# Performance work log

Measured on AMD Instinct MI355X. Metric: run time of the kernel, lower is better.

The kernel has to match this reference:

```python
import jax, jax.numpy as jnp
import numpy as np

B, C, L = 256, 500, 200
D, H, NUM_ITEMS = 64, 128, 100000
BETA = 0.7
EPS = 1e-8


def _xavier(key, fan_in, fan_out):
    lim = float(np.sqrt(6.0 / (fan_in + fan_out)))
    return jax.random.uniform(key, (fan_in, fan_out), minval=-lim, maxval=lim, dtype=jnp.float32)


def setup_inputs() -> dict:
    key = jax.random.key(0)
    ks = jax.random.split(key, 12)
    inp = {
        'candidate_items': jax.random.randint(ks[0], (B, C), 0, NUM_ITEMS, dtype=jnp.int64) if jax.config.read('jax_enable_x64') else jax.random.randint(ks[0], (B, C), 0, NUM_ITEMS),
        'query_times': jax.random.uniform(ks[1], (B,), dtype=jnp.float32),
        'candidate_histories': jax.random.uniform(ks[2], (B, C, L), dtype=jnp.float32),
        'item_emb': 0.02 * jax.random.normal(ks[3], (NUM_ITEMS, D), dtype=jnp.float32),
        'base_W1': _xavier(ks[4], D, H), 'base_b1': jnp.zeros((H,), jnp.float32),
        'base_W2': _xavier(ks[5], H, H), 'base_b2': jnp.zeros((H,), jnp.float32),
        'base_W3': _xavier(ks[6], H, 1),
        'exc_W1': _xavier(ks[7], D, H), 'exc_b1': jnp.zeros((H,), jnp.float32),
        'exc_W2': _xavier(ks[8], H, H), 'exc_b2': jnp.zeros((H,), jnp.float32),
        'exc_W3': _xavier(ks[9], H, 1),
    }
    return inp


def _mlp(x, W1, b1, W2, b2, W3):
    # (Linear + Softplus) x depth, then Linear -> 1 (no bias), squeeze last dim
    h = jax.nn.softplus(x @ W1 + b1)
    h = jax.nn.softplus(h @ W2 + b2)
    return (h @ W3)[..., 0]


def reference(candidate_items, query_times, candidate_histories, item_emb,
              base_W1, base_b1, base_W2, base_b2, base_W3,
              exc_W1, exc_b1, exc_W2, exc_b2, exc_W3):
    z = item_emb[candidate_items]                                  # [B, C, D]
    mu = jax.nn.softplus(_mlp(z, base_W1, base_b1, base_W2, base_b2, base_W3)) + EPS   # [B, C]
    alpha = jax.nn.softplus(_mlp(z, exc_W1, exc_b1, exc_W2, exc_b2, exc_W3)) + EPS     # [B, C]
    q = query_times[:, None, None]                                 # [B, 1, 1]
    mask = candidate_histories < q                                 # [B, C, L]
    delta = jnp.maximum(q - candidate_histories, 0.0)              # clamp(min=0)
    h = jnp.sum(jnp.exp(-BETA * delta) * mask, axis=-1)            # [B, C]
    return mu + alpha * h
```

## Files before the change

kernel.cpp:

```cpp
#include <hip/hip_runtime.h>
#include <math.h>

#define BB 256
#define CC 500
#define LL 200
#define DD 64
#define HH 128
#define NUM_ITEMS 100000
#define BETA 0.7f
#define EPSV 1e-8f

#define TM 32
#define WPB 4
#define NTILE (NUM_ITEMS / TM)
#define BPS 1024

typedef _Float16 half8 __attribute__((ext_vector_type(8)));
typedef float floatx4 __attribute__((ext_vector_type(4)));

__device__ __forceinline__ float softplus_safe(float x) {
    float t = __expf(-fabsf(x));
    return fmaxf(x, 0.0f) + __logf(1.0f + t);
}
__device__ __forceinline__ float softplus_fast(float x) {
    return __logf(1.0f + __expf(x));
}
__device__ __forceinline__ float softplus_small(float x) {
    float z = x * x;
    float p = fmaf(fmaf(-5.2083333e-3f, z, 0.125f), z, 0.69314718f);
    return fmaf(x, 0.5f, p);
}

__global__ __launch_bounds__(256) void prep_w(
    const float* __restrict__ W1, const float* __restrict__ W2,
    const float* __restrict__ V1, const float* __restrict__ V2,
    _Float16* __restrict__ wb)
{
    int t = blockIdx.x * 256 + threadIdx.x;
    if (t >= 49152) return;
    float v;
    if (t < 8192)       { int n = t >> 6,  k = t & 63;             v = W1[k * HH + n]; }
    else if (t < 24576) { int u = t - 8192;  int n = u >> 7, k = u & 127; v = W2[k * HH + n]; }
    else if (t < 32768) { int u = t - 24576; int n = u >> 6, k = u & 63;  v = V1[k * HH + n]; }
    else                { int u = t - 32768; int n = u >> 7, k = u & 127; v = V2[k * HH + n]; }
    wb[t] = (_Float16)v;
}

__global__ __launch_bounds__(256, 4) void mlp_mfma(
    const float* __restrict__ emb, const _Float16* __restrict__ wb,
    const float* __restrict__ b1, const float* __restrict__ b2, const float* __restrict__ W3,
    const float* __restrict__ c1, const float* __restrict__ c2, const float* __restrict__ V3,
    float* __restrict__ mu, float* __restrict__ alpha)
{
    __shared__ __align__(16) _Float16 h1s[TM * HH];
    __shared__ __align__(16) float    part[TM * WPB];
    int tid  = threadIdx.x;
    int w    = tid >> 6, lane = tid & 63;
    int quad = lane >> 4, l15 = lane & 15;

    int is_exc = blockIdx.x >= BPS;
    int bslot  = blockIdx.x - (is_exc ? BPS : 0);

    const _Float16* W1t = wb + (is_exc ? 24576 : 0);
    const _Float16* W2t = wb + (is_exc ? 32768 : 8192);
    const float* B1  = is_exc ? c1 : b1;
    const float* B2  = is_exc ? c2 : b2;
    const float* W3p = is_exc ? V3 : W3;
    float* outp = is_exc ? alpha : mu;

    half8 w1f[2][2];
    half8 w2f[4][2];
    float b1v[2], b2v[2], w3v[2];
    #pragma unroll
    for (int n = 0; n < 2; ++n) {
        int j = (2 * w + n) * 16 + l15;
        b1v[n] = B1[j];
        b2v[n] = B2[j];
        w3v[n] = W3p[j];
        #pragma unroll
        for (int kt = 0; kt < 2; ++kt)
            w1f[kt][n] = *(const half8*)(W1t + j * DD + kt * 32 + quad * 8);
        #pragma unroll
        for (int kt = 0; kt < 4; ++kt)
            w2f[kt][n] = *(const half8*)(W2t + j * HH + kt * 32 + quad * 8);
    }

    #pragma unroll 1
    for (int t = bslot; t < NTILE; t += BPS) {
        half8 zf[2][2];
        #pragma unroll
        for (int mt = 0; mt < 2; ++mt) {
            const float* p = emb + (size_t)(t * TM + mt * 16 + l15) * DD + quad * 8;
            #pragma unroll
            for (int kt = 0; kt < 2; ++kt) {
                floatx4 v0 = *(const floatx4*)(p + kt * 32);
                floatx4 v1 = *(const floatx4*)(p + kt * 32 + 4);
                half8 z;
                #pragma unroll
                for (int j = 0; j < 4; ++j) {
                    z[j] = (_Float16)v0[j]; z[4 + j] = (_Float16)v1[j];
                }
                zf[mt][kt] = z;
            }
        }

        floatx4 acc1[2][2];
        #pragma unroll
        for (int n = 0; n < 2; ++n) {
            float bv = b1v[n];
            #pragma unroll
            for (int mt = 0; mt < 2; ++mt) acc1[mt][n] = (floatx4){bv, bv, bv, bv};
        }
        #pragma unroll
        for (int kt = 0; kt < 2; ++kt)
            #pragma unroll
            for (int n = 0; n < 2; ++n)
                #pragma unroll
                for (int mt = 0; mt < 2; ++mt)
                    acc1[mt][n] = __builtin_amdgcn_mfma_f32_16x16x32_f16(zf[mt][kt], w1f[kt][n], acc1[mt][n], 0, 0, 0);
        #pragma unroll
        for (int mt = 0; mt < 2; ++mt)
            #pragma unroll
            for (int n = 0; n < 2; ++n)
                #pragma unroll
                for (int r = 0; r < 4; ++r) {
                    int itq = quad * 4 + r;
                    int sw  = ((2 * w + n) * 2 + (l15 >> 3)) ^ itq;
                    h1s[(mt * 16 + itq) * HH + sw * 8 + (l15 & 7)] =
                        (_Float16)softplus_small(acc1[mt][n][r]);
                }
        __syncthreads();

        floatx4 acc2[2][2];
        #pragma unroll
        for (int n = 0; n < 2; ++n) {
            float bv = b2v[n];
            #pragma unroll
            for (int mt = 0; mt < 2; ++mt) acc2[mt][n] = (floatx4){bv, bv, bv, bv};
        }
        #pragma unroll
        for (int kt = 0; kt < 4; ++kt) {
            half8 af[2];
            #pragma unroll
            for (int mt = 0; mt < 2; ++mt)
                af[mt] = *(const half8*)(h1s + (mt * 16 + l15) * HH + (((kt * 4 + quad) ^ l15) * 8));
            #pragma unroll
            for (int n = 0; n < 2; ++n)
                #pragma unroll
                for (int mt = 0; mt < 2; ++mt)
                    acc2[mt][n] = __builtin_amdgcn_mfma_f32_16x16x32_f16(af[mt], w2f[kt][n], acc2[mt][n], 0, 0, 0);
        }
        float sacc[2][4];
        #pragma unroll
        for (int mt = 0; mt < 2; ++mt)
            #pragma unroll
            for (int r = 0; r < 4; ++r) sacc[mt][r] = 0.0f;
        #pragma unroll
        for (int n = 0; n < 2; ++n) {
            float w3 = w3v[n];
            #pragma unroll
            for (int mt = 0; mt < 2; ++mt)
                #pragma unroll
                for (int r = 0; r < 4; ++r)
                    sacc[mt][r] += softplus_fast(acc2[mt][n][r]) * w3;
        }
        #pragma unroll
        for (int mt = 0; mt < 2; ++mt)
            #pragma unroll
            for (int r = 0; r < 4; ++r) {
                float s = sacc[mt][r];
                s += __shfl_xor(s, 1, 64);
                s += __shfl_xor(s, 2, 64);
                s += __shfl_xor(s, 4, 64);
                s += __shfl_xor(s, 8, 64);
                if (l15 == 0)
                    part[(mt * 16 + quad * 4 + r) * WPB + w] = s;
            }
        __syncthreads();

        if (tid < TM) {
            floatx4 pv = *(const floatx4*)(part + tid * WPB);
            float s = (pv[0] + pv[1]) + (pv[2] + pv[3]);
            outp[t * TM + tid] = softplus_safe(s) + EPSV;
        }
    }
}

__global__ __launch_bounds__(256) void hawkes_kernel(
    const int* __restrict__ items,
    const float* __restrict__ qt,
    const float* __restrict__ hist,
    const float* __restrict__ mu,
    const float* __restrict__ alpha,
    float* __restrict__ out)
{
    int w = blockIdx.x * 4 + (threadIdx.x >> 6);
    int lane = threadIdx.x & 63;
    float q = qt[w / CC];

    float s = 0.0f;
    if (lane < LL / 4) {
        float4 v = *(const float4*)(hist + (size_t)w * LL + lane * 4);
        s  = (v.x < q) ? __expf(BETA * v.x) : 0.f;
        s += (v.y < q) ? __expf(BETA * v.y) : 0.f;
        s += (v.z < q) ? __expf(BETA * v.z) : 0.f;
        s += (v.w < q) ? __expf(BETA * v.w) : 0.f;
    }
    #pragma unroll
    for (int off = 1; off < 64; off <<= 1) s += __shfl_xor(s, off, 64);

    if (lane == 0) {
        int it = items[w];
        out[w] = fmaf(alpha[it] * __expf(-BETA * q), s, mu[it]);
    }
}

extern "C" void kernel_launch(void* const* d_in, const int* in_sizes, int n_in,
                              void* d_out, int out_size, void* d_ws, size_t ws_size,
                              hipStream_t stream)
{
    const int*   items = (const int*)  d_in[0];
    const float* qt    = (const float*)d_in[1];
    const float* hist  = (const float*)d_in[2];
    const float* emb   = (const float*)d_in[3];
    const float* W1    = (const float*)d_in[4];
    const float* b1    = (const float*)d_in[5];
    const float* W2    = (const float*)d_in[6];
    const float* b2    = (const float*)d_in[7];
    const float* W3    = (const float*)d_in[8];
    const float* V1    = (const float*)d_in[9];
    const float* c1    = (const float*)d_in[10];
    const float* V2    = (const float*)d_in[11];
    const float* c2    = (const float*)d_in[12];
    const float* V3    = (const float*)d_in[13];

    float* out = (float*)d_out;
    _Float16* wb = (_Float16*)d_ws;
    float* mu    = (float*)((char*)d_ws + 98304);
    float* alpha = mu + NUM_ITEMS;

    prep_w<<<192, 256, 0, stream>>>(W1, W2, V1, V2, wb);

    mlp_mfma<<<2 * BPS, WPB * 64, 0, stream>>>(emb, wb, b1, b2, W3, c1, c2, V3, mu, alpha);

    hawkes_kernel<<<(BB * CC) / 4, 256, 0, stream>>>(items, qt, hist, mu, alpha, out);
}
```

Measured before the change: 240.0 us.

## Fuse both MLPs into one block and drop weight-prep kernel

Removes the separate prep_w launch that transposed and converted the weights to fp16. mlp_mfma now loads and converts the fp32 weights itself with strided loads. Each 512-thread block computes both the base and excitation MLPs on the same embedding tile, so each embedding row is read once instead of twice. The cost is a slower strided weight load in each block's prologue and more registers per thread from holding both weight sets.

```diff
diff --git a/kernel.cpp b/kernel.cpp
--- a/kernel.cpp
+++ b/kernel.cpp
@@ -11,9 +11,9 @@
 #define EPSV 1e-8f
 
 #define TM 32
-#define WPB 4
+#define WPB 8
 #define NTILE (NUM_ITEMS / TM)
-#define BPS 1024
+#define NBLK 512
 
 typedef _Float16 half8 __attribute__((ext_vector_type(8)));
 typedef float floatx4 __attribute__((ext_vector_type(4)));
@@ -31,62 +31,56 @@
     return fmaf(x, 0.5f, p);
 }
 
-__global__ __launch_bounds__(256) void prep_w(
-    const float* __restrict__ W1, const float* __restrict__ W2,
-    const float* __restrict__ V1, const float* __restrict__ V2,
-    _Float16* __restrict__ wb)
-{
-    int t = blockIdx.x * 256 + threadIdx.x;
-    if (t >= 49152) return;
-    float v;
-    if (t < 8192)       { int n = t >> 6,  k = t & 63;             v = W1[k * HH + n]; }
-    else if (t < 24576) { int u = t - 8192;  int n = u >> 7, k = u & 127; v = W2[k * HH + n]; }
-    else if (t < 32768) { int u = t - 24576; int n = u >> 6, k = u & 63;  v = V1[k * HH + n]; }
-    else                { int u = t - 32768; int n = u >> 7, k = u & 127; v = V2[k * HH + n]; }
-    wb[t] = (_Float16)v;
-}
-
-__global__ __launch_bounds__(256, 4) void mlp_mfma(
-    const float* __restrict__ emb, const _Float16* __restrict__ wb,
-    const float* __restrict__ b1, const float* __restrict__ b2, const float* __restrict__ W3,
-    const float* __restrict__ c1, const float* __restrict__ c2, const float* __restrict__ V3,
+__global__ __launch_bounds__(512, 4) void mlp_mfma(
+    const float* __restrict__ emb,
+    const float* __restrict__ W1, const float* __restrict__ b1,
+    const float* __restrict__ W2, const float* __restrict__ b2,
+    const float* __restrict__ W3,
+    const float* __restrict__ V1, const float* __restrict__ c1,
+    const float* __restrict__ V2, const float* __restrict__ c2,
+    const float* __restrict__ V3,
     float* __restrict__ mu, float* __restrict__ alpha)
 {
-    __shared__ __align__(16) _Float16 h1s[TM * HH];
-    __shared__ __align__(16) float    part[TM * WPB];
+    __shared__ __align__(16) _Float16 h1s[2][TM * HH];
+    __shared__ __align__(16) float    part[2][TM * WPB];
     int tid  = threadIdx.x;
     int w    = tid >> 6, lane = tid & 63;
     int quad = lane >> 4, l15 = lane & 15;
-
-    int is_exc = blockIdx.x >= BPS;
-    int bslot  = blockIdx.x - (is_exc ? BPS : 0);
-
-    const _Float16* W1t = wb + (is_exc ? 24576 : 0);
-    const _Float16* W2t = wb + (is_exc ? 32768 : 8192);
-    const float* B1  = is_exc ? c1 : b1;
-    const float* B2  = is_exc ? c2 : b2;
-    const float* W3p = is_exc ? V3 : W3;
-    float* outp = is_exc ? alpha : mu;
+    int j    = w * 16 + l15;
 
     half8 w1f[2][2];
-    half8 w2f[4][2];
+    half8 w2f[2][4];
     float b1v[2], b2v[2], w3v[2];
     #pragma unroll
-    for (int n = 0; n < 2; ++n) {
-        int j = (2 * w + n) * 16 + l15;
-        b1v[n] = B1[j];
-        b2v[n] = B2[j];
-        w3v[n] = W3p[j];
-        #pragma unroll
-        for (int kt = 0; kt < 2; ++kt)
-            w1f[kt][n] = *(const half8*)(W1t + j * DD + kt * 32 + quad * 8);
-        #pragma unroll
-        for (int kt = 0; kt < 4; ++kt)
-            w2f[kt][n] = *(const half8*)(W2t + j * HH + kt * 32 + quad * 8);
+    for (int s = 0; s < 2; ++s) {
+        const float* W1s = s ? V1 : W1;
+        const float* W2s = s ? V2 : W2;
+        const float* B1s = s ? c1 : b1;
+        const float* B2s = s ? c2 : b2;
+        const float* W3s = s ? V3 : W3;
+        b1v[s] = B1s[j];
+        b2v[s] = B2s[j];
+        w3v[s] = W3s[j];
+        #pragma unroll
+        for (int kt = 0; kt < 2; ++kt) {
+            half8 h;
+            #pragma unroll
+            for (int r = 0; r < 8; ++r)
+                h[r] = (_Float16)W1s[(kt * 32 + quad * 8 + r) * HH + j];
+            w1f[s][kt] = h;
+        }
+        #pragma unroll
+        for (int kt = 0; kt < 4; ++kt) {
+            half8 h;
+            #pragma unroll
+            for (int r = 0; r < 8; ++r)
+                h[r] = (_Float16)W2s[(kt * 32 + quad * 8 + r) * HH + j];
+            w2f[s][kt] = h;
+        }
     }
 
     #pragma unroll 1
-    for (int t = bslot; t < NTILE; t += BPS) {
+    for (int t = blockIdx.x; t < NTILE; t += NBLK) {
         half8 zf[2][2];
         #pragma unroll
         for (int mt = 0; mt < 2; ++mt) {
@@ -97,91 +91,76 @@
                 floatx4 v1 = *(const floatx4*)(p + kt * 32 + 4);
                 half8 z;
                 #pragma unroll
-                for (int j = 0; j < 4; ++j) {
-                    z[j] = (_Float16)v0[j]; z[4 + j] = (_Float16)v1[j];
+                for (int q = 0; q < 4; ++q) {
+                    z[q] = (_Float16)v0[q]; z[4 + q] = (_Float16)v1[q];
                 }
                 zf[mt][kt] = z;
             }
         }
 
-        floatx4 acc1[2][2];
-        #pragma unroll
-        for (int n = 0; n < 2; ++n) {
-            float bv = b1v[n];
-            #pragma unroll
-            for (int mt = 0; mt < 2; ++mt) acc1[mt][n] = (floatx4){bv, bv, bv, bv};
-        }
-        #pragma unroll
-        for (int kt = 0; kt < 2; ++kt)
-            #pragma unroll
-            for (int n = 0; n < 2; ++n)
+        #pragma unroll
+        for (int s = 0; s < 2; ++s) {
+            floatx4 acc1[2];
+            float bv = b1v[s];
+            #pragma unroll
+            for (int mt = 0; mt < 2; ++mt) acc1[mt] = (floatx4){bv, bv, bv, bv};
+            #pragma unroll
+            for (int kt = 0; kt < 2; ++kt)
                 #pragma unroll
                 for (int mt = 0; mt < 2; ++mt)
-                    acc1[mt][n] = __builtin_amdgcn_mfma_f32_16x16x32_f16(zf[mt][kt], w1f[kt][n], acc1[mt][n], 0, 0, 0);
-        #pragma unroll
-        for (int mt = 0; mt < 2; ++mt)
-            #pragma unroll
-            for (int n = 0; n < 2; ++n)
+                    acc1[mt] = __builtin_amdgcn_mfma_f32_16x16x32_f16(zf[mt][kt], w1f[s][kt], acc1[mt], 0, 0, 0);
+            #pragma unroll
+            for (int mt = 0; mt < 2; ++mt)
                 #pragma unroll
                 for (int r = 0; r < 4; ++r) {
                     int itq = quad * 4 + r;
-                    int sw  = ((2 * w + n) * 2 + (l15 >> 3)) ^ itq;
-                    h1s[(mt * 16 + itq) * HH + sw * 8 + (l15 & 7)] =
-                        (_Float16)softplus_small(acc1[mt][n][r]);
+                    int sw  = (w * 2 + (l15 >> 3)) ^ itq;
+                    h1s[s][(mt * 16 + itq) * HH + sw * 8 + (l15 & 7)] =
+                        (_Float16)softplus_small(acc1[mt][r]);
                 }
+        }
         __syncthreads();
 
-        floatx4 acc2[2][2];
-        #pragma unroll
-        for (int n = 0; n < 2; ++n) {
-            float bv = b2v[n];
-            #pragma unroll
-            for (int mt = 0; mt < 2; ++mt) acc2[mt][n] = (floatx4){bv, bv, bv, bv};
-        }
-        #pragma unroll
-        for (int kt = 0; kt < 4; ++kt) {
-            half8 af[2];
+        #pragma unroll
+        for (int s = 0; s < 2; ++s) {
+            floatx4 acc2[2];
+            float bv = b2v[s];
+            #pragma unroll
+            for (int mt = 0; mt < 2; ++mt) acc2[mt] = (floatx4){bv, bv, bv, bv};
+            #pragma unroll
+            for (int kt = 0; kt < 4; ++kt) {
+                half8 af[2];
+                #pragma unroll
+                for (int mt = 0; mt < 2; ++mt)
+                    af[mt] = *(const half8*)(h1s[s] + (mt * 16 + l15) * HH + (((kt * 4 + quad) ^ l15) * 8));
+                #pragma unroll
+                for (int mt = 0; mt < 2; ++mt)
+                    acc2[mt] = __builtin_amdgcn_mfma_f32_16x16x32_f16(af[mt], w2f[s][kt], acc2[mt], 0, 0, 0);
+            }
+            float w3 = w3v[s];
             #pragma unroll
             for (int mt = 0; mt < 2; ++mt)
-                af[mt] = *(const half8*)(h1s + (mt * 16 + l15) * HH + (((kt * 4 + quad) ^ l15) * 8));
-            #pragma unroll
-            for (int n = 0; n < 2; ++n)
-                #pragma unroll
-                for (int mt = 0; mt < 2; ++mt)
-                    acc2[mt][n] = __builtin_amdgcn_mfma_f32_16x16x32_f16(af[mt], w2f[kt][n], acc2[mt][n], 0, 0, 0);
-        }
-        float sacc[2][4];
-        #pragma unroll
-        for (int mt = 0; mt < 2; ++mt)
-            #pragma unroll
-            for (int r = 0; r < 4; ++r) sacc[mt][r] = 0.0f;
-        #pragma unroll
-        for (int n = 0; n < 2; ++n) {
-            float w3 = w3v[n];
-            #pragma unroll
-            for (int mt = 0; mt < 2; ++mt)
-                #pragma unroll
-                for (int r = 0; r < 4; ++r)
-                    sacc[mt][r] += softplus_fast(acc2[mt][n][r]) * w3;
-        }
-        #pragma unroll
-        for (int mt = 0; mt < 2; ++mt)
-            #pragma unroll
-            for (int r = 0; r < 4; ++r) {
-                float s = sacc[mt][r];
-                s += __shfl_xor(s, 1, 64);
-                s += __shfl_xor(s, 2, 64);
-                s += __shfl_xor(s, 4, 64);
-                s += __shfl_xor(s, 8, 64);
-                if (l15 == 0)
-                    part[(mt * 16 + quad * 4 + r) * WPB + w] = s;
-            }
+                #pragma unroll
+                for (int r = 0; r < 4; ++r) {
+                    float sv = softplus_fast(acc2[mt][r]) * w3;
+                    sv += __shfl_xor(sv, 1, 64);
+                    sv += __shfl_xor(sv, 2, 64);
+                    sv += __shfl_xor(sv, 4, 64);
+                    sv += __shfl_xor(sv, 8, 64);
+                    if (l15 == 0)
+                        part[s][(mt * 16 + quad * 4 + r) * WPB + w] = sv;
+                }
+        }
         __syncthreads();
 
-        if (tid < TM) {
-            floatx4 pv = *(const floatx4*)(part + tid * WPB);
-            float s = (pv[0] + pv[1]) + (pv[2] + pv[3]);
-            outp[t * TM + tid] = softplus_safe(s) + EPSV;
+        if (tid < 2 * TM) {
+            int s  = tid >> 5;
+            int it = tid & 31;
+            const float* pp = &part[s][it * WPB];
+            floatx4 a = *(const floatx4*)pp;
+            floatx4 b = *(const floatx4*)(pp + 4);
+            float sum = ((a[0] + a[1]) + (a[2] + a[3])) + ((b[0] + b[1]) + (b[2] + b[3]));
+            (s ? alpha : mu)[t * TM + it] = softplus_safe(sum) + EPSV;
         }
     }
 }
@@ -234,14 +213,12 @@
     const float* c2    = (const float*)d_in[12];
     const float* V3    = (const float*)d_in[13];
 
-    float* out = (float*)d_out;
-    _Float16* wb = (_Float16*)d_ws;
-    float* mu    = (float*)((char*)d_ws + 98304);
+    float* out   = (float*)d_out;
+    float* mu    = (float*)d_ws;
     float* alpha = mu + NUM_ITEMS;
 
-    prep_w<<<192, 256, 0, stream>>>(W1, W2, V1, V2, wb);
-
-    mlp_mfma<<<2 * BPS, WPB * 64, 0, stream>>>(emb, wb, b1, b2, W3, c1, c2, V3, mu, alpha);
+    mlp_mfma<<<NBLK, WPB * 64, 0, stream>>>(emb, W1, b1, W2, b2, W3,
+                                            V1, c1, V2, c2, V3, mu, alpha);
 
     hawkes_kernel<<<(BB * CC) / 4, 256, 0, stream>>>(items, qt, hist, mu, alpha, out);
 }
```

Result: slower. 246.7 us (+2.8%).
